# Performance work log

Measured on AMD Instinct MI355X. Metric: run time of the kernel, lower is better.

The kernel has to match this reference:

```python
import jax, jax.numpy as jnp
import numpy as np

N_NODES = 100000
N_EDGES = 800000
N_GRAPHS = 256
IN_C = 96
HID = 96
OUT_C = 16


def setup_inputs() -> dict:
    key = jax.random.key(0)
    ks = jax.random.split(key, 10)
    x = jax.random.normal(ks[0], (N_NODES, IN_C), dtype=jnp.float32)
    edge_index = jax.random.randint(ks[1], (2, N_EDGES), 0, N_NODES, dtype=jnp.int64)
    batch = jnp.sort(jax.random.randint(ks[2], (N_NODES,), 0, N_GRAPHS, dtype=jnp.int64))
    def glorot(k, fan_in, fan_out):
        s = np.sqrt(6.0 / (fan_in + fan_out)).astype(np.float32)
        return jax.random.uniform(k, (fan_in, fan_out), minval=-s, maxval=s, dtype=jnp.float32)
    W1 = glorot(ks[3], IN_C, HID)
    W2 = glorot(ks[4], HID, HID)
    W3 = glorot(ks[5], HID, HID)
    Wlin = glorot(ks[6], HID, OUT_C)
    b1 = jnp.zeros((HID,), dtype=jnp.float32)
    b2 = jnp.zeros((HID,), dtype=jnp.float32)
    b3 = jnp.zeros((HID,), dtype=jnp.float32)
    return {"x": x, "edge_index": edge_index, "batch": batch,
            "W1": W1, "b1": b1, "W2": W2, "b2": b2, "W3": W3, "b3": b3, "Wlin": Wlin}


def _gcn_conv(x, W, b, src, dst):
    # PyG GCNConv(normalize=True): add self-loops, deg includes self-loop,
    # norm_ij = deg_i^{-1/2} * deg_j^{-1/2}; linear (no bias) then scatter-add; bias after.
    n = x.shape[0]
    deg = jnp.zeros((n,), dtype=x.dtype).at[dst].add(1.0) + 1.0  # +1 self-loop
    dinv = jax.lax.rsqrt(deg)
    h = x @ W                                   # [N, H]
    coef = dinv[src] * dinv[dst]                # [E]
    msg = h[src] * coef[:, None]                # [E, H] gather
    agg = jax.ops.segment_sum(msg, dst, num_segments=n)  # scatter-add
    agg = agg + h * (dinv * dinv)[:, None]      # self-loop contribution
    return agg + b


def reference(x, edge_index, batch, W1, b1, W2, b2, W3, b3, Wlin):
    src, dst = edge_index[0], edge_index[1]
    h = jax.nn.relu(_gcn_conv(x, W1, b1, src, dst))
    h = jax.nn.relu(_gcn_conv(h, W2, b2, src, dst))
    h = _gcn_conv(h, W3, b3, src, dst)
    # global mean pool over graphs
    sums = jax.ops.segment_sum(h, batch, num_segments=N_GRAPHS)
    counts = jax.ops.segment_sum(jnp.ones((h.shape[0],), dtype=h.dtype), batch, num_segments=N_GRAPHS)
    pooled = sums / jnp.maximum(counts, 1.0)[:, None]
    return pooled @ Wlin
```

## Files before the change

### kernel.cpp

```cpp
#include <hip/hip_runtime.h>

#define NN 100000
#define NE 800000
#define NG 256
#define CH 96
#define OC 16
#define NBLK 391
#define TM 128
#define GBLK 782

typedef __attribute__((ext_vector_type(8))) short bf16x8;
typedef __attribute__((ext_vector_type(4))) float f32x4;

__device__ __forceinline__ unsigned short f2bf(float x) {
    unsigned u = __float_as_uint(x);
    return (unsigned short)((u + 0x7fffu + ((u >> 16) & 1u)) >> 16);
}
__device__ __forceinline__ float bf2f(unsigned short h) {
    return __uint_as_float(((unsigned)h) << 16);
}
__device__ __forceinline__ void split8(const float4 a, const float4 b,
                                       bf16x8& hi, bf16x8& lo) {
    float v[8] = {a.x, a.y, a.z, a.w, b.x, b.y, b.z, b.w};
#pragma unroll
    for (int j = 0; j < 8; j++) {
        unsigned short h = f2bf(v[j]);
        hi[j] = (short)h;
        lo[j] = (short)f2bf(v[j] - bf2f(h));
    }
}
__device__ __forceinline__ float4 us4_to_f4(ushort4 u) {
    return make_float4(bf2f(u.x), bf2f(u.y), bf2f(u.z), bf2f(u.w));
}
__device__ __forceinline__ void unpack8(uint4 v, float* f) {
    f[0] = __uint_as_float(v.x << 16); f[1] = __uint_as_float(v.x & 0xffff0000u);
    f[2] = __uint_as_float(v.y << 16); f[3] = __uint_as_float(v.y & 0xffff0000u);
    f[4] = __uint_as_float(v.z << 16); f[5] = __uint_as_float(v.z & 0xffff0000u);
    f[6] = __uint_as_float(v.w << 16); f[7] = __uint_as_float(v.w & 0xffff0000u);
}

__global__ __launch_bounds__(256) void k_init(int* __restrict__ cnt,
                                              const float* __restrict__ W1,
                                              const float* __restrict__ W2,
                                              const float* __restrict__ W3,
                                              unsigned short* __restrict__ WH,
                                              unsigned short* __restrict__ WL) {
    int id = blockIdx.x * 256 + threadIdx.x;
    if (id < NN + 4) cnt[id] = 0;
    if (id < 3 * CH * CH) {
        int w = id / (CH * CH);
        int r = id - w * (CH * CH);
        int k = r / CH;
        int n = r - k * CH;
        const float* Ws = (w == 0) ? W1 : (w == 1) ? W2 : W3;
        float v = Ws[k * CH + n];
        unsigned short h = f2bf(v);
        WH[w * CH * CH + n * CH + k] = h;
        WL[w * CH * CH + n * CH + k] = f2bf(v - bf2f(h));
    }
}

__global__ __launch_bounds__(256) void k_front(const float* __restrict__ X,
                                               const unsigned short* __restrict__ WH,
                                               const unsigned short* __restrict__ WL,
                                               unsigned short* __restrict__ H,
                                               const int* __restrict__ dst,
                                               int* __restrict__ cnt,
                                               int* __restrict__ slot) {
    __shared__ __align__(16) unsigned short WsH[CH * CH];
    __shared__ __align__(16) unsigned short WsL[CH * CH];

    const int tid = threadIdx.x;

    if (blockIdx.x >= GBLK) {
        int e = (blockIdx.x - GBLK) * 256 + tid;
        slot[e] = atomicAdd(&cnt[dst[e]], 1);
        return;
    }

    const int n0 = blockIdx.x * TM;
    {
        const uint4* sH = reinterpret_cast<const uint4*>(WH);
        const uint4* sL = reinterpret_cast<const uint4*>(WL);
        uint4* dH = reinterpret_cast<uint4*>(WsH);
        uint4* dL = reinterpret_cast<uint4*>(WsL);
        for (int i = tid; i < CH * CH / 8; i += 256) {
            dH[i] = sH[i];
            dL[i] = sL[i];
        }
    }
    __syncthreads();

    const int lane = tid & 63;
    const int wave = tid >> 6;
    const int lrow = lane & 15;
    const int quad = lane >> 4;

    const float4* X4 = reinterpret_cast<const float4*>(X);

    f32x4 acc[2][6];
#pragma unroll
    for (int rt = 0; rt < 2; rt++)
#pragma unroll
        for (int ct = 0; ct < 6; ct++) acc[rt][ct] = (f32x4){0.f, 0.f, 0.f, 0.f};

    int arow[2];
#pragma unroll
    for (int rt = 0; rt < 2; rt++)
        arow[rt] = min(n0 + (wave * 2 + rt) * 16 + lrow, NN - 1);

#pragma unroll
    for (int kc = 0; kc < 3; kc++) {
        bf16x8 ahi[2], alo[2];
#pragma unroll
        for (int rt = 0; rt < 2; rt++) {
            int fo = (arow[rt] * CH + kc * 32 + quad * 8) >> 2;
            split8(X4[fo], X4[fo + 1], ahi[rt], alo[rt]);
        }
#pragma unroll
        for (int ct = 0; ct < 6; ct++) {
            int bo = (ct * 16 + lrow) * CH + kc * 32 + quad * 8;
            bf16x8 bhi = *reinterpret_cast<const bf16x8*>(&WsH[bo]);
            bf16x8 blo = *reinterpret_cast<const bf16x8*>(&WsL[bo]);
#pragma unroll
            for (int rt = 0; rt < 2; rt++) {
                acc[rt][ct] = __builtin_amdgcn_mfma_f32_16x16x32_bf16(
                    alo[rt], bhi, acc[rt][ct], 0, 0, 0);
                acc[rt][ct] = __builtin_amdgcn_mfma_f32_16x16x32_bf16(
                    ahi[rt], blo, acc[rt][ct], 0, 0, 0);
                acc[rt][ct] = __builtin_amdgcn_mfma_f32_16x16x32_bf16(
                    ahi[rt], bhi, acc[rt][ct], 0, 0, 0);
            }
        }
    }

#pragma unroll
    for (int rt = 0; rt < 2; rt++) {
        int rbase = n0 + (wave * 2 + rt) * 16 + quad * 4;
#pragma unroll
        for (int ct = 0; ct < 6; ct++) {
            int col = ct * 16 + lrow;
#pragma unroll
            for (int r = 0; r < 4; r++) {
                int row = rbase + r;
                if (row < NN) H[(size_t)row * CH + col] = f2bf(acc[rt][ct][r]);
            }
        }
    }
}

__global__ __launch_bounds__(256) void k_offsets(const int* __restrict__ cnt,
                                                 int* __restrict__ gtot,
                                                 int* __restrict__ off,
                                                 float* __restrict__ dinv,
                                                 const int* __restrict__ batch,
                                                 int* __restrict__ goff) {
    int i = blockIdx.x * 256 + threadIdx.x;
    int lane = threadIdx.x & 63;
    int c = (i < NN) ? cnt[i] : 0;

    int incl = c;
#pragma unroll
    for (int d = 1; d < 64; d <<= 1) {
        int t = __shfl_up(incl, d);
        if (lane >= d) incl += t;
    }
    int total = __shfl(incl, 63);
    int base = 0;
    if (lane == 63) base = atomicAdd(gtot, total);
    base = __shfl(base, 63);

    if (i >= NN) return;
    off[i] = base + incl - c;
    dinv[i] = rsqrtf((float)c + 1.0f);
    int b = batch[i];
    int bp = (i > 0) ? batch[i - 1] : -1;
    for (int g = bp + 1; g <= b; g++) goff[g] = i;
    if (i == NN - 1)
        for (int g = b + 1; g <= NG; g++) goff[g] = NN;
}

__global__ __launch_bounds__(256) void k_build(const int* __restrict__ src,
                                               const int* __restrict__ dst,
                                               const int* __restrict__ off,
                                               const int* __restrict__ slot,
                                               const float* __restrict__ dinv,
                                               float2* __restrict__ packed) {
    int e = blockIdx.x * 256 + threadIdx.x;
    int s = src[e];
    int d = dst[e];
    packed[off[d] + slot[e]] = make_float2(__int_as_float(s), dinv[s] * dinv[d]);
}

__global__ __launch_bounds__(256) void k_gemm_bf16(const unsigned short* __restrict__ X,
                                                   const unsigned short* __restrict__ WH,
                                                   const unsigned short* __restrict__ WL,
                                                   unsigned short* __restrict__ H) {
    __shared__ __align__(16) unsigned short WsH[CH * CH];
    __shared__ __align__(16) unsigned short WsL[CH * CH];

    const int tid = threadIdx.x;
    const int n0 = blockIdx.x * TM;

    {
        const uint4* sH = reinterpret_cast<const uint4*>(WH);
        const uint4* sL = reinterpret_cast<const uint4*>(WL);
        uint4* dH = reinterpret_cast<uint4*>(WsH);
        uint4* dL = reinterpret_cast<uint4*>(WsL);
        for (int i = tid; i < CH * CH / 8; i += 256) {
            dH[i] = sH[i];
            dL[i] = sL[i];
        }
    }
    __syncthreads();

    const int lane = tid & 63;
    const int wave = tid >> 6;
    const int lrow = lane & 15;
    const int quad = lane >> 4;

    f32x4 acc[2][6];
#pragma unroll
    for (int rt = 0; rt < 2; rt++)
#pragma unroll
        for (int ct = 0; ct < 6; ct++) acc[rt][ct] = (f32x4){0.f, 0.f, 0.f, 0.f};

    int arow[2];
#pragma unroll
    for (int rt = 0; rt < 2; rt++)
        arow[rt] = min(n0 + (wave * 2 + rt) * 16 + lrow, NN - 1);

#pragma unroll
    for (int kc = 0; kc < 3; kc++) {
        bf16x8 ahi[2];
#pragma unroll
        for (int rt = 0; rt < 2; rt++)
            ahi[rt] = *reinterpret_cast<const bf16x8*>(
                &X[(size_t)arow[rt] * CH + kc * 32 + quad * 8]);
#pragma unroll
        for (int ct = 0; ct < 6; ct++) {
            int bo = (ct * 16 + lrow) * CH + kc * 32 + quad * 8;
            bf16x8 bhi = *reinterpret_cast<const bf16x8*>(&WsH[bo]);
            bf16x8 blo = *reinterpret_cast<const bf16x8*>(&WsL[bo]);
#pragma unroll
            for (int rt = 0; rt < 2; rt++) {
                acc[rt][ct] = __builtin_amdgcn_mfma_f32_16x16x32_bf16(
                    ahi[rt], blo, acc[rt][ct], 0, 0, 0);
                acc[rt][ct] = __builtin_amdgcn_mfma_f32_16x16x32_bf16(
                    ahi[rt], bhi, acc[rt][ct], 0, 0, 0);
            }
        }
    }

#pragma unroll
    for (int rt = 0; rt < 2; rt++) {
        int rbase = n0 + (wave * 2 + rt) * 16 + quad * 4;
#pragma unroll
        for (int ct = 0; ct < 6; ct++) {
            int col = ct * 16 + lrow;
#pragma unroll
            for (int r = 0; r < 4; r++) {
                int row = rbase + r;
                if (row < NN) H[(size_t)row * CH + col] = f2bf(acc[rt][ct][r]);
            }
        }
    }
}

template <bool RELU>
__global__ __launch_bounds__(256) void k_aggregate(const int* __restrict__ off,
                                                   const int* __restrict__ cnt,
                                                   const float2* __restrict__ packed,
                                                   const float* __restrict__ dinv,
                                                   const float* __restrict__ bias,
                                                   const unsigned short* __restrict__ H,
                                                   unsigned short* __restrict__ Bout) {
    int idx = blockIdx.x * 256 + threadIdx.x;
    if (idx >= NN * 12) return;
    int n = idx / 12;
    int c8 = idx - n * 12;
    int e0 = off[n];
    int e1 = e0 + cnt[n];

    const uint4* H8 = reinterpret_cast<const uint4*>(H);

    float a[8];
    {
        float hf[8];
        unpack8(H8[(size_t)n * 12 + c8], hf);
        float di = dinv[n];
        float d2 = di * di;
        const float4* bias4 = reinterpret_cast<const float4*>(bias);
        float4 b0 = bias4[c8 * 2], b1 = bias4[c8 * 2 + 1];
        float bf[8] = {b0.x, b0.y, b0.z, b0.w, b1.x, b1.y, b1.z, b1.w};
#pragma unroll
        for (int j = 0; j < 8; j++) a[j] = hf[j] * d2 + bf[j];
    }

    int e = e0;
    for (; e + 4 <= e1; e += 4) {
        float2 p0 = packed[e + 0];
        float2 p1 = packed[e + 1];
        float2 p2 = packed[e + 2];
        float2 p3 = packed[e + 3];
        uint4 v0 = H8[(size_t)__float_as_int(p0.x) * 12 + c8];
        uint4 v1 = H8[(size_t)__float_as_int(p1.x) * 12 + c8];
        uint4 v2 = H8[(size_t)__float_as_int(p2.x) * 12 + c8];
        uint4 v3 = H8[(size_t)__float_as_int(p3.x) * 12 + c8];
        float f0[8], f1[8], f2[8], f3[8];
        unpack8(v0, f0); unpack8(v1, f1); unpack8(v2, f2); unpack8(v3, f3);
#pragma unroll
        for (int j = 0; j < 8; j++)
            a[j] += f0[j] * p0.y + f1[j] * p1.y + f2[j] * p2.y + f3[j] * p3.y;
    }
    for (; e < e1; e++) {
        float2 pc = packed[e];
        uint4 v = H8[(size_t)__float_as_int(pc.x) * 12 + c8];
        float f[8];
        unpack8(v, f);
#pragma unroll
        for (int j = 0; j < 8; j++) a[j] += f[j] * pc.y;
    }
    if (RELU) {
#pragma unroll
        for (int j = 0; j < 8; j++) a[j] = fmaxf(a[j], 0.0f);
    }
    uint4 o;
    o.x = (unsigned)f2bf(a[0]) | ((unsigned)f2bf(a[1]) << 16);
    o.y = (unsigned)f2bf(a[2]) | ((unsigned)f2bf(a[3]) << 16);
    o.z = (unsigned)f2bf(a[4]) | ((unsigned)f2bf(a[5]) << 16);
    o.w = (unsigned)f2bf(a[6]) | ((unsigned)f2bf(a[7]) << 16);
    reinterpret_cast<uint4*>(Bout)[(size_t)n * 12 + c8] = o;
}

__global__ __launch_bounds__(384) void k_pool_linear(const int* __restrict__ goff,
                                                     const unsigned short* __restrict__ B,
                                                     const float* __restrict__ Wlin,
                                                     float* __restrict__ out) {
    __shared__ float4 sh[16][24];
    __shared__ float pooled[CH];
    int g = blockIdx.x;
    int t = threadIdx.x;
    int nl = t / 24;
    int c4 = t - nl * 24;
    int s = goff[g];
    int e = goff[g + 1];

    float4 acc = make_float4(0.f, 0.f, 0.f, 0.f);
    const ushort4* B4 = reinterpret_cast<const ushort4*>(B);
    for (int n = s + nl; n < e; n += 16) {
        float4 v = us4_to_f4(B4[(size_t)n * 24 + c4]);
        acc.x += v.x; acc.y += v.y; acc.z += v.z; acc.w += v.w;
    }
    sh[nl][c4] = acc;
    __syncthreads();

    if (t < 24) {
        float4 r = make_float4(0.f, 0.f, 0.f, 0.f);
#pragma unroll
        for (int j = 0; j < 16; j++) {
            float4 v = sh[j][t];
            r.x += v.x; r.y += v.y; r.z += v.z; r.w += v.w;
        }
        float inv = 1.0f / fmaxf((float)(e - s), 1.0f);
        pooled[t * 4 + 0] = r.x * inv;
        pooled[t * 4 + 1] = r.y * inv;
        pooled[t * 4 + 2] = r.z * inv;
        pooled[t * 4 + 3] = r.w * inv;
    }
    __syncthreads();

    if (t < OC) {
        float a = 0.0f;
#pragma unroll 8
        for (int k = 0; k < CH; k++) a += pooled[k] * Wlin[k * OC + t];
        out[g * OC + t] = a;
    }
}

extern "C" void kernel_launch(void* const* d_in, const int* in_sizes, int n_in,
                              void* d_out, int out_size, void* d_ws, size_t ws_size,
                              hipStream_t stream) {
    const float* x = (const float*)d_in[0];
    const int* ei = (const int*)d_in[1];
    const int* src = ei;
    const int* dst = ei + NE;
    const int* batch = (const int*)d_in[2];
    const float* W1 = (const float*)d_in[3];
    const float* b1 = (const float*)d_in[4];
    const float* W2 = (const float*)d_in[5];
    const float* b2 = (const float*)d_in[6];
    const float* W3 = (const float*)d_in[7];
    const float* b3 = (const float*)d_in[8];
    const float* Wlin = (const float*)d_in[9];
    float* out = (float*)d_out;

    char* ws = (char*)d_ws;
    unsigned short* Ha = (unsigned short*)ws;  ws += (size_t)NN * CH * 2;
    unsigned short* Hb = (unsigned short*)ws;  ws += (size_t)NN * CH * 2;
    unsigned short* Bb = (unsigned short*)ws;  ws += (size_t)NN * CH * 2;
    float2* packed = (float2*)ws;   ws += (size_t)NE * 8;
    unsigned short* WH = (unsigned short*)ws;  ws += 3 * CH * CH * 2;
    unsigned short* WL = (unsigned short*)ws;  ws += 3 * CH * CH * 2;
    float* dinv = (float*)ws;       ws += NN * 4;
    int* off = (int*)ws;            ws += NN * 4;
    int* goff = (int*)ws;           ws += 272 * 4;
    int* cnt = (int*)ws;            ws += (NN + 4) * 4;
    int* gtot = cnt + NN;
    int* slot = (int*)Bb;

    k_init<<<NBLK, 256, 0, stream>>>(cnt, W1, W2, W3, WH, WL);
    k_front<<<GBLK + NE / 256, 256, 0, stream>>>(x, WH, WL, Ha, dst, cnt, slot);
    k_offsets<<<NBLK, 256, 0, stream>>>(cnt, gtot, off, dinv, batch, goff);
    k_build<<<NE / 256, 256, 0, stream>>>(src, dst, off, slot, dinv, packed);

    const int ablk = (NN * 12 + 255) / 256;

    k_aggregate<true><<<ablk, 256, 0, stream>>>(off, cnt, packed, dinv, b1, Ha, Bb);
    k_gemm_bf16<<<GBLK, 256, 0, stream>>>(Bb, WH + CH * CH, WL + CH * CH, Hb);
    k_aggregate<true><<<ablk, 256, 0, stream>>>(off, cnt, packed, dinv, b2, Hb, Bb);
    k_gemm_bf16<<<GBLK, 256, 0, stream>>>(Bb, WH + 2 * CH * CH, WL + 2 * CH * CH, Ha);
    k_aggregate<false><<<ablk, 256, 0, stream>>>(off, cnt, packed, dinv, b3, Ha, Bb);

    k_pool_linear<<<NG, 384, 0, stream>>>(goff, Bb, Wlin, out);
}
```

Measured before the change: 308.5 us.

## Front-load histogram blocks with 4 edges each and prefetch edge records in aggregation

```diff
diff --git a/kernel.cpp b/kernel.cpp
--- a/kernel.cpp
+++ b/kernel.cpp
@@ -8,6 +8,7 @@
 #define NBLK 391
 #define TM 128
 #define GBLK 782
+#define NHIST 782
 
 typedef __attribute__((ext_vector_type(8))) short bf16x8;
 typedef __attribute__((ext_vector_type(4))) float f32x4;
@@ -72,13 +73,32 @@
 
     const int tid = threadIdx.x;
 
-    if (blockIdx.x >= GBLK) {
-        int e = (blockIdx.x - GBLK) * 256 + tid;
-        slot[e] = atomicAdd(&cnt[dst[e]], 1);
+    if (blockIdx.x < NHIST) {
+        int base = blockIdx.x * 1024 + tid;
+        if (base + 768 < NE) {
+            int d0 = dst[base];
+            int d1 = dst[base + 256];
+            int d2 = dst[base + 512];
+            int d3 = dst[base + 768];
+            int s0 = atomicAdd(&cnt[d0], 1);
+            int s1 = atomicAdd(&cnt[d1], 1);
+            int s2 = atomicAdd(&cnt[d2], 1);
+            int s3 = atomicAdd(&cnt[d3], 1);
+            slot[base] = s0;
+            slot[base + 256] = s1;
+            slot[base + 512] = s2;
+            slot[base + 768] = s3;
+        } else {
+#pragma unroll
+            for (int k = 0; k < 4; k++) {
+                int e = base + k * 256;
+                if (e < NE) slot[e] = atomicAdd(&cnt[dst[e]], 1);
+            }
+        }
         return;
     }
 
-    const int n0 = blockIdx.x * TM;
+    const int n0 = (blockIdx.x - NHIST) * TM;
     {
         const uint4* sH = reinterpret_cast<const uint4*>(WH);
         const uint4* sL = reinterpret_cast<const uint4*>(WL);
@@ -284,6 +304,15 @@
 
     const uint4* H8 = reinterpret_cast<const uint4*>(H);
 
+    int nq = (e1 - e0) >> 2;
+    float2 p0, p1, p2, p3;
+    if (nq > 0) {
+        p0 = packed[e0];
+        p1 = packed[e0 + 1];
+        p2 = packed[e0 + 2];
+        p3 = packed[e0 + 3];
+    }
+
     float a[8];
     {
         float hf[8];
@@ -298,20 +327,24 @@
     }
 
     int e = e0;
-    for (; e + 4 <= e1; e += 4) {
-        float2 p0 = packed[e + 0];
-        float2 p1 = packed[e + 1];
-        float2 p2 = packed[e + 2];
-        float2 p3 = packed[e + 3];
-        uint4 v0 = H8[(size_t)__float_as_int(p0.x) * 12 + c8];
-        uint4 v1 = H8[(size_t)__float_as_int(p1.x) * 12 + c8];
-        uint4 v2 = H8[(size_t)__float_as_int(p2.x) * 12 + c8];
-        uint4 v3 = H8[(size_t)__float_as_int(p3.x) * 12 + c8];
+    for (int q = 0; q < nq; q++) {
+        float2 c0 = p0, c1 = p1, c2 = p2, c3 = p3;
+        e += 4;
+        if (q + 1 < nq) {
+            p0 = packed[e];
+            p1 = packed[e + 1];
+            p2 = packed[e + 2];
+            p3 = packed[e + 3];
+        }
+        uint4 v0 = H8[(size_t)__float_as_int(c0.x) * 12 + c8];
+        uint4 v1 = H8[(size_t)__float_as_int(c1.x) * 12 + c8];
+        uint4 v2 = H8[(size_t)__float_as_int(c2.x) * 12 + c8];
+        uint4 v3 = H8[(size_t)__float_as_int(c3.x) * 12 + c8];
         float f0[8], f1[8], f2[8], f3[8];
         unpack8(v0, f0); unpack8(v1, f1); unpack8(v2, f2); unpack8(v3, f3);
 #pragma unroll
         for (int j = 0; j < 8; j++)
-            a[j] += f0[j] * p0.y + f1[j] * p1.y + f2[j] * p2.y + f3[j] * p3.y;
+            a[j] += f0[j] * c0.y + f1[j] * c1.y + f2[j] * c2.y + f3[j] * c3.y;
     }
     for (; e < e1; e++) {
         float2 pc = packed[e];
@@ -410,7 +443,7 @@
     int* slot = (int*)Bb;
 
     k_init<<<NBLK, 256, 0, stream>>>(cnt, W1, W2, W3, WH, WL);
-    k_front<<<GBLK + NE / 256, 256, 0, stream>>>(x, WH, WL, Ha, dst, cnt, slot);
+    k_front<<<NHIST + GBLK, 256, 0, stream>>>(x, WH, WL, Ha, dst, cnt, slot);
     k_offsets<<<NBLK, 256, 0, stream>>>(cnt, gtot, off, dinv, batch, goff);
     k_build<<<NE / 256, 256, 0, stream>>>(src, dst, off, slot, dinv, packed);
 
```

After: 316.4 us. 2.6% more time.

## Fuse final aggregation with mean-pool via per-block partial sums

Applied to the files above, without the earlier changes.

```diff
diff --git a/kernel.cpp b/kernel.cpp
--- a/kernel.cpp
+++ b/kernel.cpp
@@ -8,6 +8,7 @@
 #define NBLK 391
 #define TM 128
 #define GBLK 782
+#define ABLK 4688
 
 typedef __attribute__((ext_vector_type(8))) short bf16x8;
 typedef __attribute__((ext_vector_type(4))) float f32x4;
@@ -28,9 +29,6 @@
         hi[j] = (short)h;
         lo[j] = (short)f2bf(v[j] - bf2f(h));
     }
-}
-__device__ __forceinline__ float4 us4_to_f4(ushort4 u) {
-    return make_float4(bf2f(u.x), bf2f(u.y), bf2f(u.z), bf2f(u.w));
 }
 __device__ __forceinline__ void unpack8(uint4 v, float* f) {
     f[0] = __uint_as_float(v.x << 16); f[1] = __uint_as_float(v.x & 0xffff0000u);
@@ -44,9 +42,11 @@
                                               const float* __restrict__ W2,
                                               const float* __restrict__ W3,
                                               unsigned short* __restrict__ WH,
-                                              unsigned short* __restrict__ WL) {
+                                              unsigned short* __restrict__ WL,
+                                              float* __restrict__ fb) {
     int id = blockIdx.x * 256 + threadIdx.x;
     if (id < NN + 4) cnt[id] = 0;
+    if (id < NG * CH) fb[id] = 0.0f;
     if (id < 3 * CH * CH) {
         int w = id / (CH * CH);
         int r = id - w * (CH * CH);
@@ -333,40 +333,114 @@
     reinterpret_cast<uint4*>(Bout)[(size_t)n * 12 + c8] = o;
 }
 
-__global__ __launch_bounds__(384) void k_pool_linear(const int* __restrict__ goff,
-                                                     const unsigned short* __restrict__ B,
-                                                     const float* __restrict__ Wlin,
-                                                     float* __restrict__ out) {
-    __shared__ float4 sh[16][24];
+__global__ __launch_bounds__(256) void k_agg_pool(const int* __restrict__ off,
+                                                  const int* __restrict__ cnt,
+                                                  const float2* __restrict__ packed,
+                                                  const float* __restrict__ dinv,
+                                                  const float* __restrict__ bias,
+                                                  const unsigned short* __restrict__ H,
+                                                  const int* __restrict__ batch,
+                                                  float* __restrict__ part,
+                                                  int* __restrict__ pgid,
+                                                  float* __restrict__ fb) {
+    __shared__ float psum[4][CH];
+    const int tid = threadIdx.x;
+    for (int i = tid; i < 4 * CH; i += 256) (&psum[0][0])[i] = 0.0f;
+
+    const int idx = blockIdx.x * 256 + tid;
+    const int n0 = (blockIdx.x * 256) / 12;
+    const int g0 = batch[n0];
+    __syncthreads();
+
+    if (idx < NN * 12) {
+        int n = idx / 12;
+        int c8 = idx - n * 12;
+        int e0 = off[n];
+        int e1 = e0 + cnt[n];
+
+        const uint4* H8 = reinterpret_cast<const uint4*>(H);
+
+        float a[8];
+        {
+            float hf[8];
+            unpack8(H8[(size_t)n * 12 + c8], hf);
+            float di = dinv[n];
+            float d2 = di * di;
+            const float4* bias4 = reinterpret_cast<const float4*>(bias);
+            float4 b0 = bias4[c8 * 2], b1 = bias4[c8 * 2 + 1];
+            float bf[8] = {b0.x, b0.y, b0.z, b0.w, b1.x, b1.y, b1.z, b1.w};
+#pragma unroll
+            for (int j = 0; j < 8; j++) a[j] = hf[j] * d2 + bf[j];
+        }
+
+        int e = e0;
+        for (; e + 4 <= e1; e += 4) {
+            float2 p0 = packed[e + 0];
+            float2 p1 = packed[e + 1];
+            float2 p2 = packed[e + 2];
+            float2 p3 = packed[e + 3];
+            uint4 v0 = H8[(size_t)__float_as_int(p0.x) * 12 + c8];
+            uint4 v1 = H8[(size_t)__float_as_int(p1.x) * 12 + c8];
+            uint4 v2 = H8[(size_t)__float_as_int(p2.x) * 12 + c8];
+            uint4 v3 = H8[(size_t)__float_as_int(p3.x) * 12 + c8];
+            float f0[8], f1[8], f2[8], f3[8];
+            unpack8(v0, f0); unpack8(v1, f1); unpack8(v2, f2); unpack8(v3, f3);
+#pragma unroll
+            for (int j = 0; j < 8; j++)
+                a[j] += f0[j] * p0.y + f1[j] * p1.y + f2[j] * p2.y + f3[j] * p3.y;
+        }
+        for (; e < e1; e++) {
+            float2 pc = packed[e];
+            uint4 v = H8[(size_t)__float_as_int(pc.x) * 12 + c8];
+            float f[8];
+            unpack8(v, f);
+#pragma unroll
+            for (int j = 0; j < 8; j++) a[j] += f[j] * pc.y;
+        }
+
+        int g = batch[n];
+        int gi = g - g0;
+        if (gi < 4) {
+#pragma unroll
+            for (int j = 0; j < 8; j++) atomicAdd(&psum[gi][c8 * 8 + j], a[j]);
+        } else {
+#pragma unroll
+            for (int j = 0; j < 8; j++) atomicAdd(&fb[g * CH + c8 * 8 + j], a[j]);
+        }
+    }
+    __syncthreads();
+
+    for (int i = tid; i < 4 * CH; i += 256)
+        part[(size_t)blockIdx.x * (4 * CH) + i] = (&psum[0][0])[i];
+    if (tid < 4) pgid[blockIdx.x * 4 + tid] = g0 + tid;
+}
+
+__global__ __launch_bounds__(128) void k_pool2(const int* __restrict__ goff,
+                                               const float* __restrict__ part,
+                                               const int* __restrict__ pgid,
+                                               const float* __restrict__ fb,
+                                               const float* __restrict__ Wlin,
+                                               float* __restrict__ out) {
     __shared__ float pooled[CH];
     int g = blockIdx.x;
     int t = threadIdx.x;
-    int nl = t / 24;
-    int c4 = t - nl * 24;
     int s = goff[g];
     int e = goff[g + 1];
 
-    float4 acc = make_float4(0.f, 0.f, 0.f, 0.f);
-    const ushort4* B4 = reinterpret_cast<const ushort4*>(B);
-    for (int n = s + nl; n < e; n += 16) {
-        float4 v = us4_to_f4(B4[(size_t)n * 24 + c4]);
-        acc.x += v.x; acc.y += v.y; acc.z += v.z; acc.w += v.w;
-    }
-    sh[nl][c4] = acc;
-    __syncthreads();
-
-    if (t < 24) {
-        float4 r = make_float4(0.f, 0.f, 0.f, 0.f);
-#pragma unroll
-        for (int j = 0; j < 16; j++) {
-            float4 v = sh[j][t];
-            r.x += v.x; r.y += v.y; r.z += v.z; r.w += v.w;
-        }
-        float inv = 1.0f / fmaxf((float)(e - s), 1.0f);
-        pooled[t * 4 + 0] = r.x * inv;
-        pooled[t * 4 + 1] = r.y * inv;
-        pooled[t * 4 + 2] = r.z * inv;
-        pooled[t * 4 + 3] = r.w * inv;
+    if (t < CH) {
+        float acc = fb[g * CH + t];
+        if (e > s) {
+            int blo = (12 * s) / 256;
+            int bhi = (12 * (e - 1) + 11) / 256;
+            if (bhi > ABLK - 1) bhi = ABLK - 1;
+            for (int b = blo; b <= bhi; b++) {
+#pragma unroll
+                for (int sl = 0; sl < 4; sl++)
+                    if (pgid[b * 4 + sl] == g)
+                        acc += part[(size_t)b * (4 * CH) + sl * CH + t];
+            }
+        }
+        pooled[t] = acc / fmaxf((float)(e - s), 1.0f);
     }
     __syncthreads();
 
@@ -407,20 +481,22 @@
     int* goff = (int*)ws;           ws += 272 * 4;
     int* cnt = (int*)ws;            ws += (NN + 4) * 4;
     int* gtot = cnt + NN;
+    float* fb = (float*)ws;         ws += NG * CH * 4;
     int* slot = (int*)Bb;
-
-    k_init<<<NBLK, 256, 0, stream>>>(cnt, W1, W2, W3, WH, WL);
+    float* part = (float*)Bb;
+    int* pgid = (int*)((char*)Bb + (size_t)ABLK * 4 * CH * 4);
+
+    k_init<<<NBLK, 256, 0, stream>>>(cnt, W1, W2, W3, WH, WL, fb);
     k_front<<<GBLK + NE / 256, 256, 0, stream>>>(x, WH, WL, Ha, dst, cnt, slot);
     k_offsets<<<NBLK, 256, 0, stream>>>(cnt, gtot, off, dinv, batch, goff);
     k_build<<<NE / 256, 256, 0, stream>>>(src, dst, off, slot, dinv, packed);
 
-    const int ablk = (NN * 12 + 255) / 256;
-
-    k_aggregate<true><<<ablk, 256, 0, stream>>>(off, cnt, packed, dinv, b1, Ha, Bb);
+    k_aggregate<true><<<ABLK, 256, 0, stream>>>(off, cnt, packed, dinv, b1, Ha, Bb);
     k_gemm_bf16<<<GBLK, 256, 0, stream>>>(Bb, WH + CH * CH, WL + CH * CH, Hb);
-    k_aggregate<true><<<ablk, 256, 0, stream>>>(off, cnt, packed, dinv, b2, Hb, Bb);
+    k_aggregate<true><<<ABLK, 256, 0, stream>>>(off, cnt, packed, dinv, b2, Hb, Bb);
     k_gemm_bf16<<<GBLK, 256, 0, stream>>>(Bb, WH + 2 * CH * CH, WL + 2 * CH * CH, Ha);
-    k_aggregate<false><<<ablk, 256, 0, stream>>>(off, cnt, packed, dinv, b3, Ha, Bb);
-
-    k_pool_linear<<<NG, 384, 0, stream>>>(goff, Bb, Wlin, out);
-}
+    k_agg_pool<<<ABLK, 256, 0, stream>>>(off, cnt, packed, dinv, b3, Ha, batch,
+                                         part, pgid, fb);
+
+    k_pool2<<<NG, 128, 0, stream>>>(goff, part, pgid, fb, Wlin, out);
+}
```

Measured after the change: 342.0 us. +10.9%, slower.
